# Kernel optimization log

Hardware: AMD Instinct MI355X
Metric: run time of the kernel (lower is better)

The kernel has to match this reference:

```python
import jax, jax.numpy as jnp
import numpy as np
from jax import lax

DIM = 192
HEADS = 4

def setup_inputs() -> dict:
    key = jax.random.key(0)
    k1, k2, k3, k4 = jax.random.split(key, 4)
    x = jax.random.normal(k1, (8, DIM, 128, 128), dtype=jnp.float32)
    w_qkv = jax.random.normal(k2, (DIM * 3, DIM), dtype=jnp.float32) * 0.05
    w_dw = jax.random.normal(k3, (DIM * 3, 1, 3, 3), dtype=jnp.float32) * 0.1
    w_proj = jax.random.normal(k4, (DIM, DIM), dtype=jnp.float32) * 0.05
    temperature = jnp.ones((HEADS, 1, 1), dtype=jnp.float32)
    return {"x": x, "w_qkv": w_qkv, "w_dw": w_dw, "w_proj": w_proj, "temperature": temperature}

def _l2norm(t, eps=1e-12):
    # F.normalize(t, dim=-1): t / max(||t||_2, eps)
    n = jnp.sqrt(jnp.sum(t * t, axis=-1, keepdims=True))
    return t / jnp.maximum(n, eps)

def reference(x, w_qkv, w_dw, w_proj, temperature):
    b, c, h, w = x.shape
    heads = temperature.shape[0]
    ch = c // heads  # channels per head
    # 1x1 conv (pointwise): dim -> 3*dim
    qkv = jnp.einsum('oi,bihw->bohw', w_qkv, x)
    # 3x3 depthwise conv, groups = 3*dim, padding 1
    qkv = lax.conv_general_dilated(
        qkv, w_dw, window_strides=(1, 1), padding='SAME',
        dimension_numbers=('NCHW', 'OIHW', 'NCHW'),
        feature_group_count=3 * c)
    q, k, v = jnp.split(qkv, 3, axis=1)
    # b (head c) h w -> b head c (h w)
    q = q.reshape(b, heads, ch, h * w)
    k = k.reshape(b, heads, ch, h * w)
    v = v.reshape(b, heads, ch, h * w)
    qn = _l2norm(q)
    kn = _l2norm(k)
    # channel-channel attention: [b, head, ch, ch]
    attn = jnp.einsum('bhcn,bhdn->bhcd', qn, kn) * temperature[None]
    attn = jax.nn.relu(attn)
    out = jnp.einsum('bhcd,bhdn->bhcn', attn, v)
    out = out.reshape(b, c, h, w)
    # output 1x1 projection
    out = jnp.einsum('oi,bihw->bohw', w_proj, out)
    return out
```

## Files before the change

### kernel.cpp

```cpp
#include <hip/hip_runtime.h>

#define BB 8
#define CC 192
#define C3 576
#define HW 16384
#define HEADS 4
#define CHD 48
#define NPLANE (BB*CC)

typedef short s8v __attribute__((ext_vector_type(8)));
typedef float f16v __attribute__((ext_vector_type(16)));
typedef float f4v __attribute__((ext_vector_type(4)));

__device__ __forceinline__ ushort bfu(float f) {
    union { float f; unsigned u; } c; c.f = f;
    unsigned u = c.u + 0x7FFFu + ((c.u >> 16) & 1u);
    return (ushort)(u >> 16);
}
__device__ __forceinline__ float ubf(ushort u) {
    union { unsigned u; float f; } c; c.u = ((unsigned)u) << 16;
    return c.f;
}

__global__ void kw_cvt(const float* __restrict__ w, ushort* __restrict__ wbf) {
    int idx = blockIdx.x * 256 + threadIdx.x;
    if (idx < C3 * CC) wbf[idx] = bfu(w[idx]);
}

template<int MODE>
__global__ __launch_bounds__(256) void gemm_mfma(
    const ushort* __restrict__ A,
    const float* __restrict__ Xf,
    const ushort* __restrict__ Xh,
    ushort* __restrict__ qk, ushort* __restrict__ vb,
    float* __restrict__ outf)
{
    __shared__ ushort As[2 * 192 * 8];
    __shared__ ushort Xs[2 * 128 * 8];
    int lin = blockIdx.x, sec, pt, b;
    if (MODE == 0) {
        int logical = (lin & 7) * 384 + (lin >> 3);
        sec = logical % 3;
        int pb = logical / 3;
        pt = pb & 127; b = pb >> 7;
    } else { sec = 0; pt = lin & 127; b = lin >> 7; }
    const int t = threadIdx.x, lane = t & 63, w = t >> 6;
    const int wr = w >> 1, wc = w & 1;
    const int pbase = pt * 128;
    const ushort* Ab = A + (MODE == 0 ? (size_t)sec * CC * CC : (size_t)b * CC * CC);

    f16v acc[3][2];
    #pragma unroll
    for (int mt = 0; mt < 3; mt++)
        #pragma unroll
        for (int nt = 0; nt < 2; nt++)
            #pragma unroll
            for (int i = 0; i < 16; i++) acc[mt][nt][i] = 0.f;

    const int kgs = t >> 7, ps = t & 127;

    for (int ks = 0; ks < 12; ks++) {
        const int k0 = ks * 16;
        if (t < 192) {
            const ushort* s = Ab + (size_t)t * CC + k0;
            *(int4*)&As[(size_t)t * 8] = *(const int4*)s;
            *(int4*)&As[(size_t)(192 + t) * 8] = *(const int4*)(s + 8);
        }
        {
            unsigned wb4[4];
            if (MODE == 0) {
                const float* s = Xf + ((size_t)b * CC + k0 + kgs * 8) * HW + pbase + ps;
                float f[8];
                #pragma unroll
                for (int j = 0; j < 8; j++) f[j] = s[(size_t)j * HW];
                #pragma unroll
                for (int j = 0; j < 4; j++)
                    wb4[j] = (unsigned)bfu(f[2*j]) | ((unsigned)bfu(f[2*j+1]) << 16);
            } else {
                const ushort* s = Xh + ((size_t)b * CC + k0 + kgs * 8) * HW + pbase + ps;
                ushort u[8];
                #pragma unroll
                for (int j = 0; j < 8; j++) u[j] = s[(size_t)j * HW];
                #pragma unroll
                for (int j = 0; j < 4; j++)
                    wb4[j] = (unsigned)u[2*j] | ((unsigned)u[2*j+1] << 16);
            }
            *(int4*)&Xs[(size_t)(kgs * 128 + ps) * 8] = *(const int4*)wb4;
        }
        __syncthreads();
        const int ll = lane & 31, kg = lane >> 5;
        s8v af[3], bfv[2];
        #pragma unroll
        for (int mt = 0; mt < 3; mt++)
            af[mt] = *(const s8v*)&As[(size_t)(kg * 192 + wr * 96 + mt * 32 + ll) * 8];
        #pragma unroll
        for (int nt = 0; nt < 2; nt++)
            bfv[nt] = *(const s8v*)&Xs[(size_t)(kg * 128 + wc * 64 + nt * 32 + ll) * 8];
        #pragma unroll
        for (int mt = 0; mt < 3; mt++)
            #pragma unroll
            for (int nt = 0; nt < 2; nt++)
                acc[mt][nt] = __builtin_amdgcn_mfma_f32_32x32x16_bf16(af[mt], bfv[nt], acc[mt][nt], 0, 0, 0);
        __syncthreads();
    }

    const int ll = lane & 31, kg = lane >> 5;
    if (MODE == 0) {
        ushort* ob = sec < 2 ? qk + (size_t)(sec * BB + b) * CC * HW
                             : vb + (size_t)b * CC * HW;
        #pragma unroll
        for (int mt = 0; mt < 3; mt++)
            #pragma unroll
            for (int nt = 0; nt < 2; nt++)
                #pragma unroll
                for (int r = 0; r < 16; r++) {
                    int o = wr * 96 + mt * 32 + (r & 3) + 8 * (r >> 2) + 4 * kg;
                    int p = pbase + wc * 64 + nt * 32 + ll;
                    ob[(size_t)o * HW + p] = bfu(acc[mt][nt][r]);
                }
    } else {
        #pragma unroll
        for (int mt = 0; mt < 3; mt++)
            #pragma unroll
            for (int nt = 0; nt < 2; nt++)
                #pragma unroll
                for (int r = 0; r < 16; r++) {
                    int o = wr * 96 + mt * 32 + (r & 3) + 8 * (r >> 2) + 4 * kg;
                    int p = pbase + wc * 64 + nt * 32 + ll;
                    outf[((size_t)b * CC + o) * HW + p] = acc[mt][nt][r];
                }
    }
}

__global__ __launch_bounds__(256) void k_dw_bf(
    ushort* __restrict__ qk, ushort* __restrict__ vb,
    const float* __restrict__ wdw, float* __restrict__ sq, float* __restrict__ sk)
{
    __shared__ ushort rows[10][128];
    __shared__ float red[4];
    int pid = blockIdx.x;
    int sec = pid / NPLANE, rem = pid % NPLANE;
    int b = rem / CC, c = rem % CC;
    ushort* p = sec < 2 ? qk + ((size_t)(sec * BB + b) * CC + c) * HW
                        : vb + ((size_t)b * CC + c) * HW;
    const float* wc9 = wdw + (size_t)(sec * CC + c) * 9;
    float w0=wc9[0],w1=wc9[1],w2=wc9[2],w3=wc9[3],w4=wc9[4],w5=wc9[5],w6=wc9[6],w7=wc9[7],w8=wc9[8];
    const int t = threadIdx.x, lr = t >> 5, lx = (t & 31) * 4;
    float ss = 0.f;
    if (t < 32) ((ushort4*)rows[0])[t] = ((const ushort4*)p)[t];
    __syncthreads();
    for (int y0 = 0; y0 < 128; y0 += 8) {
        int ry = y0 + 1 + lr;
        if (ry < 128) *(ushort4*)&rows[ry % 10][lx] = *(const ushort4*)(p + (size_t)ry * 128 + lx);
        __syncthreads();
        const int oy = y0 + lr;
        float a0=0,a1=0,a2=0,a3=0;
        if (oy >= 1) {
            const ushort* rw = rows[(oy - 1) % 10];
            float m0=ubf(rw[lx]),m1=ubf(rw[lx+1]),m2=ubf(rw[lx+2]),m3=ubf(rw[lx+3]);
            float lf = lx ? ubf(rw[lx-1]) : 0.f, rt = (lx < 124) ? ubf(rw[lx+4]) : 0.f;
            a0 += w0*lf + w1*m0 + w2*m1;  a1 += w0*m0 + w1*m1 + w2*m2;
            a2 += w0*m1 + w1*m2 + w2*m3;  a3 += w0*m2 + w1*m3 + w2*rt;
        }
        {
            const ushort* rw = rows[oy % 10];
            float m0=ubf(rw[lx]),m1=ubf(rw[lx+1]),m2=ubf(rw[lx+2]),m3=ubf(rw[lx+3]);
            float lf = lx ? ubf(rw[lx-1]) : 0.f, rt = (lx < 124) ? ubf(rw[lx+4]) : 0.f;
            a0 += w3*lf + w4*m0 + w5*m1;  a1 += w3*m0 + w4*m1 + w5*m2;
            a2 += w3*m1 + w4*m2 + w5*m3;  a3 += w3*m2 + w4*m3 + w5*rt;
        }
        if (oy + 1 < 128) {
            const ushort* rw = rows[(oy + 1) % 10];
            float m0=ubf(rw[lx]),m1=ubf(rw[lx+1]),m2=ubf(rw[lx+2]),m3=ubf(rw[lx+3]);
            float lf = lx ? ubf(rw[lx-1]) : 0.f, rt = (lx < 124) ? ubf(rw[lx+4]) : 0.f;
            a0 += w6*lf + w7*m0 + w8*m1;  a1 += w6*m0 + w7*m1 + w8*m2;
            a2 += w6*m1 + w7*m2 + w8*m3;  a3 += w6*m2 + w7*m3 + w8*rt;
        }
        ss += a0*a0 + a1*a1 + a2*a2 + a3*a3;
        __syncthreads();
        ushort4 o4; o4.x = bfu(a0); o4.y = bfu(a1); o4.z = bfu(a2); o4.w = bfu(a3);
        *(ushort4*)(p + (size_t)oy * 128 + lx) = o4;
    }
    if (sec < 2) {
        for (int off = 32; off; off >>= 1) ss += __shfl_down(ss, off);
        if ((t & 63) == 0) red[t >> 6] = ss;
        __syncthreads();
        if (t == 0) (sec == 0 ? sq : sk)[b * CC + c] = red[0] + red[1] + red[2] + red[3];
    }
}

__global__ __launch_bounds__(256) void k_gram(
    const ushort* __restrict__ qk, float* __restrict__ G)
{
    int slab = blockIdx.x, h = blockIdx.y, b = blockIdx.z;
    const int t = threadIdx.x, lane = t & 63, w = t >> 6;
    const ushort* qb = qk + ((size_t)b * CC + h * CHD) * HW;
    const ushort* kb = qk + ((size_t)(BB + b) * CC + h * CHD) * HW;
    const int ll = lane & 15, lh = lane >> 4;
    f4v acc[3][3];
    #pragma unroll
    for (int i = 0; i < 3; i++)
        #pragma unroll
        for (int j = 0; j < 3; j++)
            #pragma unroll
            for (int r = 0; r < 4; r++) acc[i][j][r] = 0.f;
    const int nbase = slab * 1024 + w * 256 + lh * 8;
    for (int s = 0; s < 8; s++) {
        const int n = nbase + s * 32;
        s8v aq[3], bk[3];
        #pragma unroll
        for (int mt = 0; mt < 3; mt++)
            aq[mt] = *(const s8v*)(qb + (size_t)(mt * 16 + ll) * HW + n);
        #pragma unroll
        for (int mt = 0; mt < 3; mt++)
            bk[mt] = *(const s8v*)(kb + (size_t)(mt * 16 + ll) * HW + n);
        #pragma unroll
        for (int i = 0; i < 3; i++)
            #pragma unroll
            for (int j = 0; j < 3; j++)
                acc[i][j] = __builtin_amdgcn_mfma_f32_16x16x32_bf16(aq[i], bk[j], acc[i][j], 0, 0, 0);
    }
    float* Gb = G + (size_t)(b * HEADS + h) * CHD * CHD;
    #pragma unroll
    for (int i = 0; i < 3; i++)
        #pragma unroll
        for (int j = 0; j < 3; j++)
            #pragma unroll
            for (int r = 0; r < 4; r++) {
                int c = i * 16 + lh * 4 + r, d = j * 16 + ll;
                atomicAdd(&Gb[c * CHD + d], acc[i][j][r]);
            }
}

__global__ __launch_bounds__(256) void k_compose(
    const float* __restrict__ G, const float* __restrict__ sq, const float* __restrict__ sk,
    const float* __restrict__ temp, const float* __restrict__ wproj,
    ushort* __restrict__ Mbf)
{
    __shared__ float attnS[CHD * CHD];
    __shared__ float wS[CC * CHD];
    int h = blockIdx.x, b = blockIdx.y, t = threadIdx.x;
    float tv = temp[h];
    const float* Gb = G + (size_t)(b * HEADS + h) * CHD * CHD;
    const float* sqb = sq + b * CC + h * CHD;
    const float* skb = sk + b * CC + h * CHD;
    #pragma unroll
    for (int i = 0; i < 9; i++) {
        int idx = i * 256 + t;
        int c = idx / CHD, d = idx % CHD;
        float nq = fmaxf(sqrtf(sqb[c]), 1e-12f);
        float nk = fmaxf(sqrtf(skb[d]), 1e-12f);
        float v = Gb[idx] * tv / (nq * nk);
        attnS[idx] = fmaxf(v, 0.f);
    }
    #pragma unroll
    for (int i = 0; i < 36; i++) {
        int idx = i * 256 + t;
        wS[idx] = wproj[(idx / CHD) * CC + h * CHD + idx % CHD];
    }
    __syncthreads();
    ushort* Mb = Mbf + (size_t)b * CC * CC;
    #pragma unroll
    for (int i = 0; i < 36; i++) {
        int idx = i * 256 + t;
        int o = idx / CHD, d = idx % CHD;
        float s = 0.f;
        #pragma unroll 8
        for (int c2 = 0; c2 < CHD; c2++)
            s += wS[o * CHD + c2] * attnS[c2 * CHD + d];
        Mb[o * CC + h * CHD + d] = bfu(s);
    }
}

extern "C" void kernel_launch(void* const* d_in, const int* in_sizes, int n_in,
                              void* d_out, int out_size, void* d_ws, size_t ws_size,
                              hipStream_t stream)
{
    const float* x      = (const float*)d_in[0];
    const float* w_qkv  = (const float*)d_in[1];
    const float* w_dw   = (const float*)d_in[2];
    const float* w_proj = (const float*)d_in[3];
    const float* temp   = (const float*)d_in[4];
    float* out = (float*)d_out;
    float* ws  = (float*)d_ws;

    ushort* qk = (ushort*)d_out;

    float* G  = ws;
    float* sq = G  + (size_t)BB * HEADS * CHD * CHD;
    float* sk = sq + (size_t)BB * CC;
    ushort* wbf  = (ushort*)(sk + (size_t)BB * CC);
    ushort* Mbf  = wbf + (size_t)C3 * CC;
    ushort* vbuf = Mbf + (size_t)BB * CC * CC;

    kw_cvt<<<dim3((C3 * CC + 255) / 256), 256, 0, stream>>>(w_qkv, wbf);
    hipMemsetAsync(G, 0, (size_t)BB * HEADS * CHD * CHD * sizeof(float), stream);

    gemm_mfma<0><<<dim3(3072), 256, 0, stream>>>(wbf, x, nullptr, qk, vbuf, nullptr);

    k_dw_bf<<<dim3(3 * NPLANE), 256, 0, stream>>>(qk, vbuf, w_dw, sq, sk);

    k_gram<<<dim3(16, HEADS, BB), 256, 0, stream>>>(qk, G);

    k_compose<<<dim3(HEADS, BB), 256, 0, stream>>>(G, sq, sk, temp, w_proj, Mbf);

    gemm_mfma<1><<<dim3(1024), 256, 0, stream>>>(Mbf, nullptr, vbuf, nullptr, nullptr, out);
}
```

Baseline: 445.5 us.

## Pre-transpose GEMM inputs to k-packed bf16 layout and stage outputs via LDS

Adds a transpose kernel that converts x (and later v) into a bf16 layout packed 8 along k per pixel, so each MFMA fragment can be loaded straight from global memory without LDS staging or per-iteration syncs. The MODE 0 epilogue now writes results to LDS first and then stores coalesced 16-byte rows, instead of scattered 2-byte stores. The projection GEMM grid is also remapped with the same XCD-style swizzle. In exchange it adds two extra full-tensor transpose passes through memory and a larger workspace.

```diff
diff --git a/kernel.cpp b/kernel.cpp
--- a/kernel.cpp
+++ b/kernel.cpp
@@ -27,27 +27,57 @@
     if (idx < C3 * CC) wbf[idx] = bfu(w[idx]);
 }
 
+template<int SRC>
+__global__ __launch_bounds__(256) void k_trans(
+    const float* __restrict__ xf, const ushort* __restrict__ xh,
+    ushort* __restrict__ T)
+{
+    const int b = blockIdx.x, cg = blockIdx.y;
+    const int p = blockIdx.z * 1024 + threadIdx.x * 4;
+    float a[8][4];
+    #pragma unroll
+    for (int c = 0; c < 8; c++) {
+        if (SRC == 0) {
+            *(float4*)a[c] = *(const float4*)(xf + ((size_t)(b * CC + cg * 8 + c) * HW + p));
+        } else {
+            ushort4 u = *(const ushort4*)(xh + ((size_t)(b * CC + cg * 8 + c) * HW + p));
+            a[c][0] = ubf(u.x); a[c][1] = ubf(u.y); a[c][2] = ubf(u.z); a[c][3] = ubf(u.w);
+        }
+    }
+    #pragma unroll
+    for (int j = 0; j < 4; j++) {
+        unsigned wp[4];
+        #pragma unroll
+        for (int i = 0; i < 4; i++)
+            wp[i] = (unsigned)bfu(a[2*i][j]) | ((unsigned)bfu(a[2*i+1][j]) << 16);
+        *(uint4*)(T + ((size_t)(b * 24 + cg) * HW + p + j) * 8) = *(const uint4*)wp;
+    }
+}
+
 template<int MODE>
 __global__ __launch_bounds__(256) void gemm_mfma(
     const ushort* __restrict__ A,
-    const float* __restrict__ Xf,
-    const ushort* __restrict__ Xh,
-    ushort* __restrict__ qk, ushort* __restrict__ vb,
+    const ushort* __restrict__ BT,
+    ushort* __restrict__ qk, ushort* __restrict__ vpl,
     float* __restrict__ outf)
 {
-    __shared__ ushort As[2 * 192 * 8];
-    __shared__ ushort Xs[2 * 128 * 8];
+    __shared__ ushort Rep[MODE == 0 ? 192 * 136 : 8];
     int lin = blockIdx.x, sec, pt, b;
     if (MODE == 0) {
         int logical = (lin & 7) * 384 + (lin >> 3);
         sec = logical % 3;
         int pb = logical / 3;
         pt = pb & 127; b = pb >> 7;
-    } else { sec = 0; pt = lin & 127; b = lin >> 7; }
+    } else {
+        int logical = (lin & 7) * 128 + (lin >> 3);
+        sec = 0; b = logical >> 7; pt = logical & 127;
+    }
     const int t = threadIdx.x, lane = t & 63, w = t >> 6;
     const int wr = w >> 1, wc = w & 1;
+    const int ll = lane & 31, kg = lane >> 5;
     const int pbase = pt * 128;
-    const ushort* Ab = A + (MODE == 0 ? (size_t)sec * CC * CC : (size_t)b * CC * CC);
+    const ushort* Ab = A + (size_t)(MODE == 0 ? sec : b) * CC * CC;
+    const ushort* Bb = BT + (size_t)b * 24 * HW * 8;
 
     f16v acc[3][2];
     #pragma unroll
@@ -57,67 +87,43 @@
             #pragma unroll
             for (int i = 0; i < 16; i++) acc[mt][nt][i] = 0.f;
 
-    const int kgs = t >> 7, ps = t & 127;
-
+    #pragma unroll 4
     for (int ks = 0; ks < 12; ks++) {
-        const int k0 = ks * 16;
-        if (t < 192) {
-            const ushort* s = Ab + (size_t)t * CC + k0;
-            *(int4*)&As[(size_t)t * 8] = *(const int4*)s;
-            *(int4*)&As[(size_t)(192 + t) * 8] = *(const int4*)(s + 8);
-        }
-        {
-            unsigned wb4[4];
-            if (MODE == 0) {
-                const float* s = Xf + ((size_t)b * CC + k0 + kgs * 8) * HW + pbase + ps;
-                float f[8];
-                #pragma unroll
-                for (int j = 0; j < 8; j++) f[j] = s[(size_t)j * HW];
-                #pragma unroll
-                for (int j = 0; j < 4; j++)
-                    wb4[j] = (unsigned)bfu(f[2*j]) | ((unsigned)bfu(f[2*j+1]) << 16);
-            } else {
-                const ushort* s = Xh + ((size_t)b * CC + k0 + kgs * 8) * HW + pbase + ps;
-                ushort u[8];
-                #pragma unroll
-                for (int j = 0; j < 8; j++) u[j] = s[(size_t)j * HW];
-                #pragma unroll
-                for (int j = 0; j < 4; j++)
-                    wb4[j] = (unsigned)u[2*j] | ((unsigned)u[2*j+1] << 16);
-            }
-            *(int4*)&Xs[(size_t)(kgs * 128 + ps) * 8] = *(const int4*)wb4;
-        }
-        __syncthreads();
-        const int ll = lane & 31, kg = lane >> 5;
-        s8v af[3], bfv[2];
-        #pragma unroll
-        for (int mt = 0; mt < 3; mt++)
-            af[mt] = *(const s8v*)&As[(size_t)(kg * 192 + wr * 96 + mt * 32 + ll) * 8];
+        s8v af[3], bfr[2];
+        #pragma unroll
+        for (int mt = 0; mt < 3; mt++)
+            af[mt] = *(const s8v*)(Ab + (size_t)(wr * 96 + mt * 32 + ll) * CC + ks * 16 + kg * 8);
         #pragma unroll
         for (int nt = 0; nt < 2; nt++)
-            bfv[nt] = *(const s8v*)&Xs[(size_t)(kg * 128 + wc * 64 + nt * 32 + ll) * 8];
+            bfr[nt] = *(const s8v*)(Bb + ((size_t)(ks * 2 + kg) * HW + pbase + wc * 64 + nt * 32 + ll) * 8);
         #pragma unroll
         for (int mt = 0; mt < 3; mt++)
             #pragma unroll
             for (int nt = 0; nt < 2; nt++)
-                acc[mt][nt] = __builtin_amdgcn_mfma_f32_32x32x16_bf16(af[mt], bfv[nt], acc[mt][nt], 0, 0, 0);
-        __syncthreads();
-    }
-
-    const int ll = lane & 31, kg = lane >> 5;
+                acc[mt][nt] = __builtin_amdgcn_mfma_f32_32x32x16_bf16(af[mt], bfr[nt], acc[mt][nt], 0, 0, 0);
+    }
+
     if (MODE == 0) {
-        ushort* ob = sec < 2 ? qk + (size_t)(sec * BB + b) * CC * HW
-                             : vb + (size_t)b * CC * HW;
         #pragma unroll
         for (int mt = 0; mt < 3; mt++)
             #pragma unroll
             for (int nt = 0; nt < 2; nt++)
                 #pragma unroll
-                for (int r = 0; r < 16; r++) {
-                    int o = wr * 96 + mt * 32 + (r & 3) + 8 * (r >> 2) + 4 * kg;
-                    int p = pbase + wc * 64 + nt * 32 + ll;
-                    ob[(size_t)o * HW + p] = bfu(acc[mt][nt][r]);
-                }
+                for (int g = 0; g < 4; g++)
+                    #pragma unroll
+                    for (int j = 0; j < 4; j++)
+                        Rep[(wr * 96 + mt * 32 + 8 * g + 4 * kg + j) * 136
+                            + wc * 64 + nt * 32 + ll] = bfu(acc[mt][nt][4 * g + j]);
+        __syncthreads();
+        ushort* ob = (sec == 2) ? vpl + (size_t)b * CC * HW
+                                : qk + (size_t)(sec * BB + b) * CC * HW;
+        #pragma unroll
+        for (int i = 0; i < 12; i++) {
+            int idx = i * 256 + t;
+            int row = idx >> 4, c8 = idx & 15;
+            int4 vv = *(const int4*)&Rep[row * 136 + c8 * 8];
+            *(int4*)(ob + (size_t)row * HW + pbase + c8 * 8) = vv;
+        }
     } else {
         #pragma unroll
         for (int mt = 0; mt < 3; mt++)
@@ -282,27 +288,31 @@
     const float* w_proj = (const float*)d_in[3];
     const float* temp   = (const float*)d_in[4];
     float* out = (float*)d_out;
-    float* ws  = (float*)d_ws;
 
     ushort* qk = (ushort*)d_out;
 
-    float* G  = ws;
-    float* sq = G  + (size_t)BB * HEADS * CHD * CHD;
-    float* sk = sq + (size_t)BB * CC;
-    ushort* wbf  = (ushort*)(sk + (size_t)BB * CC);
-    ushort* Mbf  = wbf + (size_t)C3 * CC;
-    ushort* vbuf = Mbf + (size_t)BB * CC * CC;
+    ushort* xT = (ushort*)d_ws;
+    ushort* vb = xT + (size_t)BB * CC * HW;
+    float*  G  = (float*)(vb + (size_t)BB * CC * HW);
+    float*  sq = G + (size_t)BB * HEADS * CHD * CHD;
+    float*  sk = sq + (size_t)BB * CC;
+    ushort* wbf = (ushort*)(sk + (size_t)BB * CC);
+    ushort* Mbf = wbf + (size_t)C3 * CC;
 
     kw_cvt<<<dim3((C3 * CC + 255) / 256), 256, 0, stream>>>(w_qkv, wbf);
     hipMemsetAsync(G, 0, (size_t)BB * HEADS * CHD * CHD * sizeof(float), stream);
 
-    gemm_mfma<0><<<dim3(3072), 256, 0, stream>>>(wbf, x, nullptr, qk, vbuf, nullptr);
-
-    k_dw_bf<<<dim3(3 * NPLANE), 256, 0, stream>>>(qk, vbuf, w_dw, sq, sk);
+    k_trans<0><<<dim3(BB, 24, 16), 256, 0, stream>>>(x, nullptr, xT);
+
+    gemm_mfma<0><<<dim3(3072), 256, 0, stream>>>(wbf, xT, qk, vb, nullptr);
+
+    k_dw_bf<<<dim3(3 * NPLANE), 256, 0, stream>>>(qk, vb, w_dw, sq, sk);
+
+    k_trans<1><<<dim3(BB, 24, 16), 256, 0, stream>>>(nullptr, vb, xT);
 
     k_gram<<<dim3(16, HEADS, BB), 256, 0, stream>>>(qk, G);
 
     k_compose<<<dim3(HEADS, BB), 256, 0, stream>>>(G, sq, sk, temp, w_proj, Mbf);
 
-    gemm_mfma<1><<<dim3(1024), 256, 0, stream>>>(Mbf, nullptr, vbuf, nullptr, nullptr, out);
-}
+    gemm_mfma<1><<<dim3(1024), 256, 0, stream>>>(Mbf, xT, nullptr, nullptr, out);
+}
```

Measured after the change: 425.8 us. -4.4%, faster.
